# Performance work log

Measured on AMD Instinct MI355X. Metric: run time of the kernel, lower is better.

The kernel has to match this reference:

```python
import jax, jax.numpy as jnp
import numpy as np

EPS = 1e-5
KH = KW = 3
PAD = 1

def conv3x3(x, w, b=None):
    out = jax.lax.conv_general_dilated(
        x, w, window_strides=(1, 1), padding=((PAD, PAD), (PAD, PAD)),
        dimension_numbers=("NCHW", "OIHW", "NCHW"))
    if b is not None:
        out = out + b[None, :, None, None]
    return out

def batchnorm(x, gamma, beta):
    # training-mode BatchNorm2d: batch statistics over (N, H, W)
    mean = x.mean(axis=(0, 2, 3), keepdims=True)
    var = x.var(axis=(0, 2, 3), keepdims=True)
    return gamma[None, :, None, None] * (x - mean) / jnp.sqrt(var + EPS) + beta[None, :, None, None]

def bilinear_gather(x, y_pos, x_pos):
    # x: [B,C,H,W]; y_pos/x_pos: [B,P,H,W] (P = KH*KW sampling taps)
    # zero padding outside image (mmcv modulated deform conv semantics)
    B, C, H, W = x.shape
    P = y_pos.shape[1]
    x_flat = x.reshape(B, C, H * W)
    y0 = jnp.floor(y_pos)
    x0 = jnp.floor(x_pos)
    ly = y_pos - y0
    lx = x_pos - x0
    out = jnp.zeros((B, C, P, H, W), dtype=x.dtype)
    for dy, dx, wgt in ((0, 0, (1 - ly) * (1 - lx)), (0, 1, (1 - ly) * lx),
                        (1, 0, ly * (1 - lx)), (1, 1, ly * lx)):
        yi = y0 + dy
        xi = x0 + dx
        valid = ((yi >= 0) & (yi <= H - 1) & (xi >= 0) & (xi <= W - 1)).astype(x.dtype)
        yc = jnp.clip(yi, 0, H - 1).astype(jnp.int32)
        xc = jnp.clip(xi, 0, W - 1).astype(jnp.int32)
        idx = (yc * W + xc).reshape(B, 1, P * H * W)
        vals = jnp.take_along_axis(x_flat, jnp.broadcast_to(idx, (B, C, P * H * W)), axis=2)
        vals = vals.reshape(B, C, P, H, W)
        out = out + vals * (wgt * valid)[:, None]
    return out  # [B,C,P,H,W]

def modulated_deform_conv(x, w_off, b_off, w_dcn):
    B, C, H, W = x.shape
    P = KH * KW
    off = conv3x3(x, w_off, b_off)  # [B, 3*P, H, W]
    o1, o2, m = jnp.split(off, 3, axis=1)
    offset = jnp.concatenate([o1, o2], axis=1)            # [B, 2P, H, W]
    offset = offset.reshape(B, P, 2, H, W)                # channel 2p -> dy, 2p+1 -> dx
    mask = jax.nn.sigmoid(m)                              # [B, P, H, W]
    hh = jnp.arange(H, dtype=x.dtype)
    ww = jnp.arange(W, dtype=x.dtype)
    ky = jnp.arange(KH, dtype=x.dtype)
    kx = jnp.arange(KW, dtype=x.dtype)
    # base sampling grid per tap p = ky*KW + kx: (h - PAD + ky, w - PAD + kx)
    base_y = (hh[None, :] - PAD + ky[:, None])            # [KH, H]
    base_x = (ww[None, :] - PAD + kx[:, None])            # [KW, W]
    base_y = jnp.broadcast_to(base_y[:, None, :, None], (KH, KW, H, W)).reshape(P, H, W)
    base_x = jnp.broadcast_to(base_x[None, :, None, :], (KH, KW, H, W)).reshape(P, H, W)
    y_pos = base_y[None] + offset[:, :, 0]                # [B,P,H,W]
    x_pos = base_x[None] + offset[:, :, 1]
    sampled = bilinear_gather(x, y_pos, x_pos)            # [B,C,P,H,W]
    sampled = sampled * mask[:, None]
    w = w_dcn.reshape(w_dcn.shape[0], C, P)               # [O, C, P]
    return jnp.einsum("bcphw,ocp->bohw", sampled, w)

def setup_inputs() -> dict:
    key = jax.random.key(0)
    ks = jax.random.split(key, 10)
    B, Ch, H, W = 4, 256, 64, 64
    Cin, Cout = 2 * Ch, 256
    P = KH * KW
    inp = {
        "input_v": jax.random.normal(ks[0], (B, Ch, H, W), jnp.float32),
        "input_i": jax.random.normal(ks[1], (B, Ch, H, W), jnp.float32),
        "w_off": jax.random.normal(ks[2], (3 * P, Cin, KH, KW), jnp.float32) * 0.01,
        "b_off": jnp.zeros((3 * P,), jnp.float32),
        "w_dcn": jax.random.normal(ks[3], (Cout, Cin, KH, KW), jnp.float32) * (1.0 / np.sqrt(Cin * P)),
        "gamma1": jnp.ones((Cout,), jnp.float32),
        "beta1": jnp.zeros((Cout,), jnp.float32),
        "w2": jax.random.normal(ks[4], (Cout, Cout, KH, KW), jnp.float32) * (1.0 / np.sqrt(Cout * P)),
        "gamma2": jnp.ones((Cout,), jnp.float32),
        "beta2": jnp.zeros((Cout,), jnp.float32),
    }
    return inp

def reference(input_v, input_i, w_off, b_off, w_dcn, gamma1, beta1, w2, gamma2, beta2):
    x = jnp.concatenate([input_v, input_i], axis=1)
    out = modulated_deform_conv(x, w_off, b_off, w_dcn)
    out = jax.nn.relu(batchnorm(out, gamma1, beta1))
    out = jax.nn.relu(batchnorm(conv3x3(out, w2), gamma2, beta2))
    return out
```

## Files before the change

kernel.cpp:

```cpp
#include <hip/hip_runtime.h>
#include <cstdint>
#include <cstddef>

typedef unsigned short u16;
typedef __attribute__((ext_vector_type(8))) short s16x8;
typedef __attribute__((ext_vector_type(4))) float f32x4;

#define DEV __device__ __forceinline__

DEV float bf2f(short u){
  union { unsigned int i; float f; } v;
  v.i = ((unsigned int)(u16)u) << 16;
  return v.f;
}
DEV short f2bf(float f){
  union { float f; unsigned int i; } v; v.f = f;
  unsigned int u = v.i;
  u += 0x7fffu + ((u >> 16) & 1u);
  return (short)(u >> 16);
}
DEV s16x8 s16x8_zero(){
  s16x8 z;
#pragma unroll
  for(int j=0;j<8;j++) z[j]=0;
  return z;
}
DEV f32x4 f32x4_zero(){
  f32x4 z;
#pragma unroll
  for(int j=0;j<4;j++) z[j]=0.f;
  return z;
}
DEV f32x4 mfma16(s16x8 a, s16x8 b, f32x4 c){
  return __builtin_amdgcn_mfma_f32_16x16x32_bf16(a, b, c, 0, 0, 0);
}
DEV void cp16(const void* g, void* l){
  __builtin_amdgcn_global_load_lds(
      (const __attribute__((address_space(1))) unsigned int*)g,
      (__attribute__((address_space(3))) unsigned int*)l, 16, 0, 0);
}

static constexpr size_t OFF_ACC_B   = 0;
static constexpr size_t OUT1_ACC_B  = 2097152;
static constexpr size_t OUT2_ACC_B  = 18874368;
static constexpr size_t STATS_B     = 35651584;
static constexpr size_t ZERO_BYTES  = 35655680;
static constexpr size_t XN_PAD_B    = 35655680;
static constexpr size_t OUT1N_PAD_B = 53497856;
static constexpr size_t WOFFT_B     = 62418944;
static constexpr size_t WDCNT_B     = 62713856;
static constexpr size_t W2T_B       = 65073152;
static constexpr size_t SAMP_O_B    = 66252800;
static constexpr size_t SAMP_W_B    = 68612096;

__global__ void k_border(u16* __restrict__ xp, u16* __restrict__ op){
  const int cid = blockIdx.x, t = threadIdx.x;
  const int b = cid / 260, rem = cid % 260;
  int y, x;
  if(rem < 132){ y = (rem/66)*65; x = rem%66; }
  else { int r2 = rem-132; x = (r2>>6)*65; y = 1 + (r2&63); }
  const size_t cell = (size_t)(b*66+y)*66 + x;
  ((unsigned int*)(xp + cell*512))[t] = 0;
  if(t < 128) ((unsigned int*)(op + cell*256))[t] = 0;
}

__global__ void k_x_to_nhwc(const float* __restrict__ v, const float* __restrict__ vi,
                            u16* __restrict__ xn){
  __shared__ float tile[64][65];
  const int b = blockIdx.z, c0 = blockIdx.y*64, h = blockIdx.x;
  const float* src = (c0 < 256) ? (v  + ((size_t)b*256 + c0)      *4096)
                                : (vi + ((size_t)b*256 + (c0-256))*4096);
  const int t = threadIdx.x;
#pragma unroll
  for(int k=0;k<16;k++){
    int idx = t + k*256;
    int cl = idx >> 6, wl = idx & 63;
    tile[cl][wl] = src[(size_t)cl*4096 + h*64 + wl];
  }
  __syncthreads();
#pragma unroll
  for(int k=0;k<16;k++){
    int idx = t + k*256;
    int wl = idx >> 6, cl = idx & 63;
    xn[((size_t)(b*66 + h+1)*66 + (wl+1))*512 + c0 + cl] = (u16)f2bf(tile[cl][wl]);
  }
}

__global__ void k_prep_woff(const float* __restrict__ w, u16* __restrict__ wt){
  int idx = blockIdx.x*256 + threadIdx.x;
  if(idx >= 32*4608) return;
  int n = idx / 4608, k = idx % 4608;
  int t = k >> 9, c = k & 511;
  float val = (n < 27) ? w[(size_t)(n*512 + c)*9 + t] : 0.f;
  wt[idx] = (u16)f2bf(val);
}
__global__ void k_prep_wdcn(const float* __restrict__ w, u16* __restrict__ wt){
  int idx = blockIdx.x*256 + threadIdx.x;
  if(idx >= 256*4608) return;
  int n = idx / 4608, k = idx % 4608;
  int t = k >> 9, c = k & 511;
  wt[idx] = (u16)f2bf(w[(size_t)(n*512 + c)*9 + t]);
}
__global__ void k_prep_w2(const float* __restrict__ w, u16* __restrict__ wt){
  int idx = blockIdx.x*256 + threadIdx.x;
  if(idx >= 256*2304) return;
  int n = idx / 2304, k = idx % 2304;
  int t = k >> 8, c = k & 255;
  wt[idx] = (u16)f2bf(w[(size_t)(n*256 + c)*9 + t]);
}

__global__ __launch_bounds__(256, 4) void k_conv_off(
    const u16* __restrict__ xn, const u16* __restrict__ wt, float* __restrict__ offa){
  __shared__ short A_lds[8][64][8];
  __shared__ short B_lds[8][32][8];
  const int tid = threadIdx.x;
  const int lane = tid & 63, wid = tid >> 6;
  const int quad = lane >> 4, ln = lane & 15;
  const int m0 = blockIdx.x * 64;
  const int b = m0 >> 12;
  const int h = (m0 >> 6) & 63;
  const int ks = blockIdx.y;
  const int m_base = wid * 16;
  const s16x8* Ap = (const s16x8*)A_lds;
  const s16x8* Bp = (const s16x8*)B_lds;
  f32x4 acc[2];
  acc[0] = f32x4_zero(); acc[1] = f32x4_zero();

  for(int tpi=0; tpi<3; tpi++){
    const int tp = ks*3 + tpi;
    const int ty = tp/3, tx = tp - ty*3;
    const u16* arow = xn + ((size_t)(b*66 + h+ty)*66 + lane + tx)*512;
    const u16* brow = wt + (size_t)(lane & 31)*4608 + tp*512 + (wid*2 + (lane>>5))*8;
    for(int s=0; s<8; s++){
      const int cb = s*64;
      cp16(arow + cb + (wid*2)*8,     &A_lds[wid*2][0][0]);
      cp16(arow + cb + (wid*2+1)*8,   &A_lds[wid*2+1][0][0]);
      cp16(brow + cb,                 &B_lds[wid*2][0][0]);
      __syncthreads();
#pragma unroll
      for(int cc=0; cc<2; cc++){
        const int s2 = cc*4 + quad;
        s16x8 a  = Ap[s2*64 + m_base + ln];
        s16x8 b0 = Bp[s2*32 + ln];
        s16x8 b1 = Bp[s2*32 + 16 + ln];
        acc[0] = mfma16(a, b0, acc[0]);
        acc[1] = mfma16(a, b1, acc[1]);
      }
      __syncthreads();
    }
  }
#pragma unroll
  for(int nf=0;nf<2;nf++){
    const int col = nf*16 + ln;
#pragma unroll
    for(int i=0;i<4;i++){
      const int row = m_base + quad*4 + i;
      unsafeAtomicAdd(offa + (size_t)(m0+row)*32 + col, acc[nf][i]);
    }
  }
}

__global__ void k_sampler(const float* __restrict__ offa, const float* __restrict__ boff,
                          int* __restrict__ so, float* __restrict__ sw){
  const int idx = blockIdx.x*256 + threadIdx.x;
  if(idx >= 16384*9) return;
  const int m = idx / 9, tp = idx - m*9;
  const int b = m >> 12, h = (m >> 6) & 63, w = m & 63;
  const float* orow = offa + (size_t)m*32;
  float dy = orow[2*tp]   + boff[2*tp];
  float dx = orow[2*tp+1] + boff[2*tp+1];
  float mz = orow[18+tp]  + boff[18+tp];
  float mk = 1.f / (1.f + expf(-mz));
  float ypos = (float)(h - 1 + tp/3) + dy;
  float xpos = (float)(w - 1 + tp%3) + dx;
  float y0f = floorf(ypos), x0f = floorf(xpos);
  float ly = ypos - y0f, lx = xpos - x0f;
  int y0 = (int)y0f, x0 = (int)x0f;
#pragma unroll
  for(int k=0;k<4;k++){
    int ddy = k >> 1, ddx = k & 1;
    int yi = y0 + ddy, xi = x0 + ddx;
    bool vv = (yi >= 0) & (yi < 64) & (xi >= 0) & (xi < 64);
    float wk = (ddy ? ly : 1.f-ly) * (ddx ? lx : 1.f-lx) * mk;
    if(!vv) wk = 0.f;
    int yc = yi < 0 ? 0 : (yi > 63 ? 63 : yi);
    int xc = xi < 0 ? 0 : (xi > 63 ? 63 : xi);
    so[(size_t)idx*4 + k] = ((b*66 + yc+1)*66 + xc+1) << 9;
    sw[(size_t)idx*4 + k] = wk;
  }
}

__global__ __launch_bounds__(256, 3) void k_dcn(
    const u16* __restrict__ xn, const u16* __restrict__ wt,
    const int* __restrict__ so, const float* __restrict__ sw,
    float* __restrict__ outa){
  __shared__ short A_lds[8][64][8];
  __shared__ short B_lds[8][256][8];
  const int tid = threadIdx.x;
  const int lane = tid & 63, wid = tid >> 6;
  const int quad = lane >> 4, ln = lane & 15;
  const int m0 = blockIdx.x * 64;
  const int ks = blockIdx.y;
  const int m_base = (wid >> 1)*32, n_base = (wid & 1)*128;
  const int r = tid >> 2, sub = tid & 3;
  const int nw = wid * 64;
  const s16x8* Ap = (const s16x8*)A_lds;
  const s16x8* Bp = (const s16x8*)B_lds;
  f32x4 acc[2][8];
#pragma unroll
  for(int mf=0;mf<2;mf++)
#pragma unroll
    for(int nf=0;nf<8;nf++) acc[mf][nf] = f32x4_zero();

  for(int tpi=0; tpi<3; tpi++){
    const int tp = ks*3 + tpi;
    const int4   po = *(const int4*)  (so + ((size_t)(m0+r)*9 + tp)*4);
    const float4 pw = *(const float4*)(sw + ((size_t)(m0+r)*9 + tp)*4);
    const u16* a0p = xn + po.x + sub*8;
    const u16* a1p = xn + po.y + sub*8;
    const u16* a2p = xn + po.z + sub*8;
    const u16* a3p = xn + po.w + sub*8;
    const u16* bsrc = wt + (size_t)(nw + lane)*4608 + tp*512;

    for(int s=0; s<8; s++){
      const int c0 = s*64;
      s16x8 v00 = *(const s16x8*)(a0p + c0);
      s16x8 v01 = *(const s16x8*)(a1p + c0);
      s16x8 v02 = *(const s16x8*)(a2p + c0);
      s16x8 v03 = *(const s16x8*)(a3p + c0);
      s16x8 v10 = *(const s16x8*)(a0p + c0 + 32);
      s16x8 v11 = *(const s16x8*)(a1p + c0 + 32);
      s16x8 v12 = *(const s16x8*)(a2p + c0 + 32);
      s16x8 v13 = *(const s16x8*)(a3p + c0 + 32);
#pragma unroll
      for(int s2=0; s2<8; s2++)
        cp16(bsrc + c0 + s2*8, &B_lds[s2][nw][0]);
      s16x8 pk0, pk1;
#pragma unroll
      for(int j=0;j<8;j++){
        float f0 = pw.x * bf2f(v00[j]);
        f0 = fmaf(pw.y, bf2f(v01[j]), f0);
        f0 = fmaf(pw.z, bf2f(v02[j]), f0);
        f0 = fmaf(pw.w, bf2f(v03[j]), f0);
        pk0[j] = f2bf(f0);
        float f1 = pw.x * bf2f(v10[j]);
        f1 = fmaf(pw.y, bf2f(v11[j]), f1);
        f1 = fmaf(pw.z, bf2f(v12[j]), f1);
        f1 = fmaf(pw.w, bf2f(v13[j]), f1);
        pk1[j] = f2bf(f1);
      }
      *(s16x8*)(&A_lds[sub][r][0])     = pk0;
      *(s16x8*)(&A_lds[sub+4][r][0])   = pk1;
      __syncthreads();
#pragma unroll
      for(int cc=0; cc<2; cc++){
        const int s2 = cc*4 + quad;
        s16x8 a0 = Ap[s2*64 + m_base + ln];
        s16x8 a1 = Ap[s2*64 + m_base + 16 + ln];
        s16x8 bfr[8];
#pragma unroll
        for(int nf=0;nf<8;nf++) bfr[nf] = Bp[s2*256 + n_base + nf*16 + ln];
#pragma unroll
        for(int nf=0;nf<8;nf++){
          acc[0][nf] = mfma16(a0, bfr[nf], acc[0][nf]);
          acc[1][nf] = mfma16(a1, bfr[nf], acc[1][nf]);
        }
      }
      __syncthreads();
    }
  }
#pragma unroll
  for(int mf=0;mf<2;mf++)
#pragma unroll
    for(int nf=0;nf<8;nf++){
      const int col = n_base + nf*16 + ln;
#pragma unroll
      for(int i=0;i<4;i++){
        const int row = m_base + mf*16 + quad*4 + i;
        unsafeAtomicAdd(outa + (size_t)(m0+row)*256 + col, acc[mf][nf][i]);
      }
    }
}

__global__ __launch_bounds__(256, 3) void k_conv2(
    const u16* __restrict__ a_in, const u16* __restrict__ wt, float* __restrict__ outa){
  __shared__ short A_lds[8][64][8];
  __shared__ short B_lds[8][256][8];
  const int tid = threadIdx.x;
  const int lane = tid & 63, wid = tid >> 6;
  const int quad = lane >> 4, ln = lane & 15;
  const int m0 = blockIdx.x * 64;
  const int b = m0 >> 12;
  const int h = (m0 >> 6) & 63;
  const int ks = blockIdx.y;
  const int m_base = (wid >> 1)*32, n_base = (wid & 1)*128;
  const int nw = wid * 64;
  const s16x8* Ap = (const s16x8*)A_lds;
  const s16x8* Bp = (const s16x8*)B_lds;
  f32x4 acc[2][8];
#pragma unroll
  for(int mf=0;mf<2;mf++)
#pragma unroll
    for(int nf=0;nf<8;nf++) acc[mf][nf] = f32x4_zero();

  for(int tpi=0; tpi<3; tpi++){
    const int tp = ks*3 + tpi;
    const int ty = tp/3, tx = tp - ty*3;
    const u16* arow = a_in + ((size_t)(b*66 + h+ty)*66 + lane + tx)*256;
    const u16* bsrc = wt + (size_t)(nw + lane)*2304 + tp*256;
    for(int s=0; s<4; s++){
      const int c0 = s*64;
      cp16(arow + c0 + wid*8,       &A_lds[wid][0][0]);
      cp16(arow + c0 + (wid+4)*8,   &A_lds[wid+4][0][0]);
#pragma unroll
      for(int s2=0; s2<8; s2++)
        cp16(bsrc + c0 + s2*8, &B_lds[s2][nw][0]);
      __syncthreads();
#pragma unroll
      for(int cc=0; cc<2; cc++){
        const int s2 = cc*4 + quad;
        s16x8 a0 = Ap[s2*64 + m_base + ln];
        s16x8 a1 = Ap[s2*64 + m_base + 16 + ln];
        s16x8 bfr[8];
#pragma unroll
        for(int nf=0;nf<8;nf++) bfr[nf] = Bp[s2*256 + n_base + nf*16 + ln];
#pragma unroll
        for(int nf=0;nf<8;nf++){
          acc[0][nf] = mfma16(a0, bfr[nf], acc[0][nf]);
          acc[1][nf] = mfma16(a1, bfr[nf], acc[1][nf]);
        }
      }
      __syncthreads();
    }
  }
#pragma unroll
  for(int mf=0;mf<2;mf++)
#pragma unroll
    for(int nf=0;nf<8;nf++){
      const int col = n_base + nf*16 + ln;
#pragma unroll
      for(int i=0;i<4;i++){
        const int row = m_base + mf*16 + quad*4 + i;
        unsafeAtomicAdd(outa + (size_t)(m0+row)*256 + col, acc[mf][nf][i]);
      }
    }
}

__global__ void k_stats(const float* __restrict__ acc, float* __restrict__ sum,
                        float* __restrict__ sq){
  const int m0 = blockIdx.x*64;
  const int c = threadIdx.x;
  float s = 0.f, q = 0.f;
  for(int i=0;i<64;i++){
    float v = acc[(size_t)(m0+i)*256 + c];
    s += v; q += v*v;
  }
  unsafeAtomicAdd(sum + c, s);
  unsafeAtomicAdd(sq + c, q);
}

__global__ void k_bn1(const float* __restrict__ acc, const float* __restrict__ sum,
                      const float* __restrict__ sq, const float* __restrict__ g,
                      const float* __restrict__ bt, u16* __restrict__ o){
  __shared__ float sc[256], sh[256];
  const int t = threadIdx.x;
  {
    float mean = sum[t] * (1.f/16384.f);
    float var  = sq[t] * (1.f/16384.f) - mean*mean;
    float rstd = rsqrtf(var + 1e-5f);
    float s = g[t] * rstd;
    sc[t] = s; sh[t] = bt[t] - mean*s;
  }
  __syncthreads();
  const int c4 = (t & 63) * 4;
  const float s0 = sc[c4], s1 = sc[c4+1], s2 = sc[c4+2], s3 = sc[c4+3];
  const float h0 = sh[c4], h1 = sh[c4+1], h2 = sh[c4+2], h3 = sh[c4+3];
#pragma unroll
  for(int k=0;k<4;k++){
    int m = blockIdx.x*16 + k*4 + (t>>6);
    int b = m >> 12, hh = (m >> 6) & 63, ww = m & 63;
    const float4 v = *(const float4*)(acc + (size_t)m*256 + c4);
    unsigned int lo = (unsigned int)(u16)f2bf(fmaxf(0.f, v.x*s0 + h0))
                    | ((unsigned int)(u16)f2bf(fmaxf(0.f, v.y*s1 + h1)) << 16);
    unsigned int hi = (unsigned int)(u16)f2bf(fmaxf(0.f, v.z*s2 + h2))
                    | ((unsigned int)(u16)f2bf(fmaxf(0.f, v.w*s3 + h3)) << 16);
    uint2 pr; pr.x = lo; pr.y = hi;
    *(uint2*)(o + ((size_t)(b*66 + hh+1)*66 + ww+1)*256 + c4) = pr;
  }
}

__global__ void k_bn2_out(const float* __restrict__ acc, const float* __restrict__ sum,
                          const float* __restrict__ sq, const float* __restrict__ g,
                          const float* __restrict__ bt, float* __restrict__ out){
  __shared__ float tile[64][65];
  __shared__ float sc[64], sh[64];
  const int t = threadIdx.x;
  const int b = blockIdx.z, c0 = blockIdx.y*64, hw0 = blockIdx.x*64;
  if(t < 64){
    int c = c0 + t;
    float mean = sum[c] * (1.f/16384.f);
    float var  = sq[c] * (1.f/16384.f) - mean*mean;
    float rstd = rsqrtf(var + 1e-5f);
    float s = g[c] * rstd;
    sc[t] = s; sh[t] = bt[c] - mean*s;
  }
  __syncthreads();
#pragma unroll
  for(int k=0;k<16;k++){
    int idx = t + k*256;
    int wl = idx >> 6, cl = idx & 63;
    float v = acc[(size_t)((b<<12) + hw0 + wl)*256 + c0 + cl];
    tile[wl][cl] = fmaxf(0.f, v*sc[cl] + sh[cl]);
  }
  __syncthreads();
#pragma unroll
  for(int k=0;k<16;k++){
    int idx = t + k*256;
    int cl = idx >> 6, wl = idx & 63;
    out[(size_t)(b*256 + c0 + cl)*4096 + hw0 + wl] = tile[wl][cl];
  }
}

extern "C" void kernel_launch(void* const* d_in, const int* in_sizes, int n_in,
                              void* d_out, int out_size, void* d_ws, size_t ws_size,
                              hipStream_t stream){
  const float* in_v  = (const float*)d_in[0];
  const float* in_i  = (const float*)d_in[1];
  const float* w_off = (const float*)d_in[2];
  const float* b_off = (const float*)d_in[3];
  const float* w_dcn = (const float*)d_in[4];
  const float* g1    = (const float*)d_in[5];
  const float* bt1   = (const float*)d_in[6];
  const float* w2    = (const float*)d_in[7];
  const float* g2    = (const float*)d_in[8];
  const float* bt2   = (const float*)d_in[9];
  float* out = (float*)d_out;
  char* ws = (char*)d_ws;

  float* off_acc  = (float*)(ws + OFF_ACC_B);
  float* out1_acc = (float*)(ws + OUT1_ACC_B);
  float* out2_acc = (float*)(ws + OUT2_ACC_B);
  float* stats    = (float*)(ws + STATS_B);
  float* sum1 = stats,       *sq1 = stats + 256;
  float* sum2 = stats + 512, *sq2 = stats + 768;
  u16* xn_pad    = (u16*)(ws + XN_PAD_B);
  u16* out1n_pad = (u16*)(ws + OUT1N_PAD_B);
  u16* wofft = (u16*)(ws + WOFFT_B);
  u16* wdcnt = (u16*)(ws + WDCNT_B);
  u16* w2t   = (u16*)(ws + W2T_B);
  int*   samp_o = (int*)(ws + SAMP_O_B);
  float* samp_w = (float*)(ws + SAMP_W_B);

  hipMemsetAsync(ws, 0, ZERO_BYTES, stream);
  k_border<<<1040, 256, 0, stream>>>(xn_pad, out1n_pad);
  k_x_to_nhwc<<<dim3(64,8,4), 256, 0, stream>>>(in_v, in_i, xn_pad);
  k_prep_woff<<<576, 256, 0, stream>>>(w_off, wofft);
  k_prep_wdcn<<<4608, 256, 0, stream>>>(w_dcn, wdcnt);
  k_prep_w2<<<2304, 256, 0, stream>>>(w2, w2t);
  k_conv_off<<<dim3(256,3), 256, 0, stream>>>(xn_pad, wofft, off_acc);
  k_sampler<<<576, 256, 0, stream>>>(off_acc, b_off, samp_o, samp_w);
  k_dcn<<<dim3(256,3), 256, 0, stream>>>(xn_pad, wdcnt, samp_o, samp_w, out1_acc);
  k_stats<<<256, 256, 0, stream>>>(out1_acc, sum1, sq1);
  k_bn1<<<1024, 256, 0, stream>>>(out1_acc, sum1, sq1, g1, bt1, out1n_pad);
  k_conv2<<<dim3(256,3), 256, 0, stream>>>(out1n_pad, w2t, out2_acc);
  k_stats<<<256, 256, 0, stream>>>(out2_acc, sum2, sq2);
  k_bn2_out<<<dim3(64,4,4), 256, 0, stream>>>(out2_acc, sum2, sq2, g2, bt2, out);
}
```

Baseline: 411.1 us.

## Double-buffer LDS in conv GEMMs, retile weights, split K into six slices

The three implicit-GEMM conv kernels (offset conv, deformable conv, conv2) now use ping-pong LDS buffers with a 32-channel K step. The next tile's global loads and bilinear gather are issued before the current tile's MFMAs, cutting the barriers per step from two to one. Weights are pre-permuted into a K-chunk-major, N-contiguous layout so each B tile is one contiguous copy. The K split doubles from 3 to 6 grid slices and the occupancy hints rise. In exchange there are more atomic adds into the fp32 accumulators and more register pressure from keeping prefetched gather values live.

```diff
diff --git a/kernel.cpp b/kernel.cpp
--- a/kernel.cpp
+++ b/kernel.cpp
@@ -18,12 +18,6 @@
   unsigned int u = v.i;
   u += 0x7fffu + ((u >> 16) & 1u);
   return (short)(u >> 16);
-}
-DEV s16x8 s16x8_zero(){
-  s16x8 z;
-#pragma unroll
-  for(int j=0;j<8;j++) z[j]=0;
-  return z;
 }
 DEV f32x4 f32x4_zero(){
   f32x4 z;
@@ -87,75 +81,82 @@
 }
 
 __global__ void k_prep_woff(const float* __restrict__ w, u16* __restrict__ wt){
-  int idx = blockIdx.x*256 + threadIdx.x;
-  if(idx >= 32*4608) return;
-  int n = idx / 4608, k = idx % 4608;
-  int t = k >> 9, c = k & 511;
-  float val = (n < 27) ? w[(size_t)(n*512 + c)*9 + t] : 0.f;
-  wt[idx] = (u16)f2bf(val);
+  int i = blockIdx.x*256 + threadIdx.x;
+  if(i >= 147456) return;
+  int j = i & 7, n = (i>>3) & 31, kcp = i>>8;
+  int kc = kcp & 63, tp = kcp >> 6;
+  int c = kc*8 + j;
+  float val = (n < 27) ? w[(size_t)(n*512 + c)*9 + tp] : 0.f;
+  wt[i] = (u16)f2bf(val);
 }
 __global__ void k_prep_wdcn(const float* __restrict__ w, u16* __restrict__ wt){
-  int idx = blockIdx.x*256 + threadIdx.x;
-  if(idx >= 256*4608) return;
-  int n = idx / 4608, k = idx % 4608;
-  int t = k >> 9, c = k & 511;
-  wt[idx] = (u16)f2bf(w[(size_t)(n*512 + c)*9 + t]);
+  int i = blockIdx.x*256 + threadIdx.x;
+  if(i >= 1179648) return;
+  int j = i & 7, n = (i>>3) & 255, kcp = i>>11;
+  int kc = kcp & 63, tp = kcp >> 6;
+  int c = kc*8 + j;
+  wt[i] = (u16)f2bf(w[(size_t)(n*512 + c)*9 + tp]);
 }
 __global__ void k_prep_w2(const float* __restrict__ w, u16* __restrict__ wt){
-  int idx = blockIdx.x*256 + threadIdx.x;
-  if(idx >= 256*2304) return;
-  int n = idx / 2304, k = idx % 2304;
-  int t = k >> 8, c = k & 255;
-  wt[idx] = (u16)f2bf(w[(size_t)(n*256 + c)*9 + t]);
-}
-
-__global__ __launch_bounds__(256, 4) void k_conv_off(
+  int i = blockIdx.x*256 + threadIdx.x;
+  if(i >= 589824) return;
+  int j = i & 7, n = (i>>3) & 255, kcp = i>>11;
+  int kc = kcp & 31, tp = kcp >> 5;
+  int c = kc*8 + j;
+  wt[i] = (u16)f2bf(w[(size_t)(n*256 + c)*9 + tp]);
+}
+
+__global__ __launch_bounds__(256, 6) void k_conv_off(
     const u16* __restrict__ xn, const u16* __restrict__ wt, float* __restrict__ offa){
-  __shared__ short A_lds[8][64][8];
-  __shared__ short B_lds[8][32][8];
+  __shared__ short A[2][4][64][8];
+  __shared__ short B[2][4][32][8];
   const int tid = threadIdx.x;
   const int lane = tid & 63, wid = tid >> 6;
   const int quad = lane >> 4, ln = lane & 15;
   const int m0 = blockIdx.x * 64;
-  const int b = m0 >> 12;
-  const int h = (m0 >> 6) & 63;
-  const int ks = blockIdx.y;
+  const int b = m0 >> 12, h = (m0 >> 6) & 63;
+  const int gst0 = blockIdx.y * 24;
   const int m_base = wid * 16;
-  const s16x8* Ap = (const s16x8*)A_lds;
-  const s16x8* Bp = (const s16x8*)B_lds;
-  f32x4 acc[2];
-  acc[0] = f32x4_zero(); acc[1] = f32x4_zero();
-
-  for(int tpi=0; tpi<3; tpi++){
-    const int tp = ks*3 + tpi;
+  f32x4 acc0 = f32x4_zero(), acc1 = f32x4_zero();
+
+  {
+    const int tp = gst0 >> 4, s = gst0 & 15;
     const int ty = tp/3, tx = tp - ty*3;
-    const u16* arow = xn + ((size_t)(b*66 + h+ty)*66 + lane + tx)*512;
-    const u16* brow = wt + (size_t)(lane & 31)*4608 + tp*512 + (wid*2 + (lane>>5))*8;
-    for(int s=0; s<8; s++){
-      const int cb = s*64;
-      cp16(arow + cb + (wid*2)*8,     &A_lds[wid*2][0][0]);
-      cp16(arow + cb + (wid*2+1)*8,   &A_lds[wid*2+1][0][0]);
-      cp16(brow + cb,                 &B_lds[wid*2][0][0]);
-      __syncthreads();
-#pragma unroll
-      for(int cc=0; cc<2; cc++){
-        const int s2 = cc*4 + quad;
-        s16x8 a  = Ap[s2*64 + m_base + ln];
-        s16x8 b0 = Bp[s2*32 + ln];
-        s16x8 b1 = Bp[s2*32 + 16 + ln];
-        acc[0] = mfma16(a, b0, acc[0]);
-        acc[1] = mfma16(a, b1, acc[1]);
-      }
-      __syncthreads();
-    }
+    cp16(xn + ((size_t)(b*66 + h+ty)*66 + lane + tx)*512 + s*32 + wid*8, &A[0][wid][0][0]);
+    if(wid < 2)
+      cp16(wt + ((size_t)tp*64 + s*4)*256 + wid*512 + lane*8, (short*)&B[0][0][0][0] + wid*512);
+  }
+  __syncthreads();
+
+  int buf = 0;
+  for(int it=0; it<24; it++){
+    const int nb = buf ^ 1;
+    if(it < 23){
+      const int gn = gst0 + it + 1;
+      const int tp = gn >> 4, s = gn & 15;
+      const int ty = tp/3, tx = tp - ty*3;
+      cp16(xn + ((size_t)(b*66 + h+ty)*66 + lane + tx)*512 + s*32 + wid*8, &A[nb][wid][0][0]);
+      if(wid < 2)
+        cp16(wt + ((size_t)tp*64 + s*4)*256 + wid*512 + lane*8, (short*)&B[nb][0][0][0] + wid*512);
+    }
+    const s16x8* Ap = (const s16x8*)&A[buf][0][0][0];
+    const s16x8* Bp = (const s16x8*)&B[buf][0][0][0];
+    s16x8 a  = Ap[quad*64 + m_base + ln];
+    s16x8 b0 = Bp[quad*32 + ln];
+    s16x8 b1 = Bp[quad*32 + 16 + ln];
+    acc0 = mfma16(a, b0, acc0);
+    acc1 = mfma16(a, b1, acc1);
+    __syncthreads();
+    buf = nb;
   }
 #pragma unroll
   for(int nf=0;nf<2;nf++){
+    const f32x4 v = nf ? acc1 : acc0;
     const int col = nf*16 + ln;
 #pragma unroll
     for(int i=0;i<4;i++){
       const int row = m_base + quad*4 + i;
-      unsafeAtomicAdd(offa + (size_t)(m0+row)*32 + col, acc[nf][i]);
+      unsafeAtomicAdd(offa + (size_t)(m0+row)*32 + col, v[i]);
     }
   }
 }
@@ -190,84 +191,100 @@
   }
 }
 
-__global__ __launch_bounds__(256, 3) void k_dcn(
+__global__ __launch_bounds__(256, 4) void k_dcn(
     const u16* __restrict__ xn, const u16* __restrict__ wt,
     const int* __restrict__ so, const float* __restrict__ sw,
     float* __restrict__ outa){
-  __shared__ short A_lds[8][64][8];
-  __shared__ short B_lds[8][256][8];
+  __shared__ short A[2][4][64][8];
+  __shared__ short B[2][4][256][8];
   const int tid = threadIdx.x;
   const int lane = tid & 63, wid = tid >> 6;
   const int quad = lane >> 4, ln = lane & 15;
   const int m0 = blockIdx.x * 64;
-  const int ks = blockIdx.y;
+  const int gst0 = blockIdx.y * 24;
   const int m_base = (wid >> 1)*32, n_base = (wid & 1)*128;
   const int r = tid >> 2, sub = tid & 3;
-  const int nw = wid * 64;
-  const s16x8* Ap = (const s16x8*)A_lds;
-  const s16x8* Bp = (const s16x8*)B_lds;
   f32x4 acc[2][8];
 #pragma unroll
   for(int mf=0;mf<2;mf++)
 #pragma unroll
     for(int nf=0;nf<8;nf++) acc[mf][nf] = f32x4_zero();
 
-  for(int tpi=0; tpi<3; tpi++){
-    const int tp = ks*3 + tpi;
-    const int4   po = *(const int4*)  (so + ((size_t)(m0+r)*9 + tp)*4);
-    const float4 pw = *(const float4*)(sw + ((size_t)(m0+r)*9 + tp)*4);
-    const u16* a0p = xn + po.x + sub*8;
-    const u16* a1p = xn + po.y + sub*8;
-    const u16* a2p = xn + po.z + sub*8;
-    const u16* a3p = xn + po.w + sub*8;
-    const u16* bsrc = wt + (size_t)(nw + lane)*4608 + tp*512;
-
-    for(int s=0; s<8; s++){
-      const int c0 = s*64;
-      s16x8 v00 = *(const s16x8*)(a0p + c0);
-      s16x8 v01 = *(const s16x8*)(a1p + c0);
-      s16x8 v02 = *(const s16x8*)(a2p + c0);
-      s16x8 v03 = *(const s16x8*)(a3p + c0);
-      s16x8 v10 = *(const s16x8*)(a0p + c0 + 32);
-      s16x8 v11 = *(const s16x8*)(a1p + c0 + 32);
-      s16x8 v12 = *(const s16x8*)(a2p + c0 + 32);
-      s16x8 v13 = *(const s16x8*)(a3p + c0 + 32);
-#pragma unroll
-      for(int s2=0; s2<8; s2++)
-        cp16(bsrc + c0 + s2*8, &B_lds[s2][nw][0]);
-      s16x8 pk0, pk1;
+  int4 po; float4 pw;
+  s16x8 g0, g1, g2, g3;
+
+  {
+    const int tp = gst0 >> 4, s = gst0 & 15;
+    po = *(const int4*)  (so + ((size_t)(m0+r)*9 + tp)*4);
+    pw = *(const float4*)(sw + ((size_t)(m0+r)*9 + tp)*4);
+    const u16* bs = wt + ((size_t)tp*64 + s*4)*2048 + (wid*4)*512 + lane*8;
+    short* bd = (short*)&B[0][0][0][0] + (wid*4)*512;
+#pragma unroll
+    for(int i=0;i<4;i++) cp16(bs + i*512, bd + i*512);
+    const int c0 = s*32 + sub*8;
+    g0 = *(const s16x8*)(xn + po.x + c0);
+    g1 = *(const s16x8*)(xn + po.y + c0);
+    g2 = *(const s16x8*)(xn + po.z + c0);
+    g3 = *(const s16x8*)(xn + po.w + c0);
+    s16x8 pk;
+#pragma unroll
+    for(int j=0;j<8;j++){
+      float f = pw.x * bf2f(g0[j]);
+      f = fmaf(pw.y, bf2f(g1[j]), f);
+      f = fmaf(pw.z, bf2f(g2[j]), f);
+      f = fmaf(pw.w, bf2f(g3[j]), f);
+      pk[j] = f2bf(f);
+    }
+    *(s16x8*)(&A[0][sub][r][0]) = pk;
+  }
+  __syncthreads();
+
+  int buf = 0;
+  for(int it=0; it<24; it++){
+    const int nb = buf ^ 1;
+    if(it < 23){
+      const int gn = gst0 + it + 1;
+      const int tp = gn >> 4, s = gn & 15;
+      if((gn & 15) == 0){
+        po = *(const int4*)  (so + ((size_t)(m0+r)*9 + tp)*4);
+        pw = *(const float4*)(sw + ((size_t)(m0+r)*9 + tp)*4);
+      }
+      const u16* bs = wt + ((size_t)tp*64 + s*4)*2048 + (wid*4)*512 + lane*8;
+      short* bd = (short*)&B[nb][0][0][0] + (wid*4)*512;
+#pragma unroll
+      for(int i=0;i<4;i++) cp16(bs + i*512, bd + i*512);
+      const int c0 = s*32 + sub*8;
+      g0 = *(const s16x8*)(xn + po.x + c0);
+      g1 = *(const s16x8*)(xn + po.y + c0);
+      g2 = *(const s16x8*)(xn + po.z + c0);
+      g3 = *(const s16x8*)(xn + po.w + c0);
+    }
+    {
+      const s16x8* Ap = (const s16x8*)&A[buf][0][0][0];
+      const s16x8* Bp = (const s16x8*)&B[buf][0][0][0];
+      s16x8 a0 = Ap[quad*64 + m_base + ln];
+      s16x8 a1 = Ap[quad*64 + m_base + 16 + ln];
+#pragma unroll
+      for(int nf=0;nf<8;nf++){
+        s16x8 bf = Bp[quad*256 + n_base + nf*16 + ln];
+        acc[0][nf] = mfma16(a0, bf, acc[0][nf]);
+        acc[1][nf] = mfma16(a1, bf, acc[1][nf]);
+      }
+    }
+    if(it < 23){
+      s16x8 pk;
 #pragma unroll
       for(int j=0;j<8;j++){
-        float f0 = pw.x * bf2f(v00[j]);
-        f0 = fmaf(pw.y, bf2f(v01[j]), f0);
-        f0 = fmaf(pw.z, bf2f(v02[j]), f0);
-        f0 = fmaf(pw.w, bf2f(v03[j]), f0);
-        pk0[j] = f2bf(f0);
-        float f1 = pw.x * bf2f(v10[j]);
-        f1 = fmaf(pw.y, bf2f(v11[j]), f1);
-        f1 = fmaf(pw.z, bf2f(v12[j]), f1);
-        f1 = fmaf(pw.w, bf2f(v13[j]), f1);
-        pk1[j] = f2bf(f1);
+        float f = pw.x * bf2f(g0[j]);
+        f = fmaf(pw.y, bf2f(g1[j]), f);
+        f = fmaf(pw.z, bf2f(g2[j]), f);
+        f = fmaf(pw.w, bf2f(g3[j]), f);
+        pk[j] = f2bf(f);
       }
-      *(s16x8*)(&A_lds[sub][r][0])     = pk0;
-      *(s16x8*)(&A_lds[sub+4][r][0])   = pk1;
-      __syncthreads();
-#pragma unroll
-      for(int cc=0; cc<2; cc++){
-        const int s2 = cc*4 + quad;
-        s16x8 a0 = Ap[s2*64 + m_base + ln];
-        s16x8 a1 = Ap[s2*64 + m_base + 16 + ln];
-        s16x8 bfr[8];
-#pragma unroll
-        for(int nf=0;nf<8;nf++) bfr[nf] = Bp[s2*256 + n_base + nf*16 + ln];
-#pragma unroll
-        for(int nf=0;nf<8;nf++){
-          acc[0][nf] = mfma16(a0, bfr[nf], acc[0][nf]);
-          acc[1][nf] = mfma16(a1, bfr[nf], acc[1][nf]);
-        }
-      }
-      __syncthreads();
-    }
+      *(s16x8*)(&A[nb][sub][r][0]) = pk;
+    }
+    __syncthreads();
+    buf = nb;
   }
 #pragma unroll
   for(int mf=0;mf<2;mf++)
@@ -282,56 +299,59 @@
     }
 }
 
-__global__ __launch_bounds__(256, 3) void k_conv2(
+__global__ __launch_bounds__(256, 4) void k_conv2(
     const u16* __restrict__ a_in, const u16* __restrict__ wt, float* __restrict__ outa){
-  __shared__ short A_lds[8][64][8];
-  __shared__ short B_lds[8][256][8];
+  __shared__ short A[2][4][64][8];
+  __shared__ short B[2][4][256][8];
   const int tid = threadIdx.x;
   const int lane = tid & 63, wid = tid >> 6;
   const int quad = lane >> 4, ln = lane & 15;
   const int m0 = blockIdx.x * 64;
-  const int b = m0 >> 12;
-  const int h = (m0 >> 6) & 63;
-  const int ks = blockIdx.y;
+  const int b = m0 >> 12, h = (m0 >> 6) & 63;
+  const int gst0 = blockIdx.y * 12;
   const int m_base = (wid >> 1)*32, n_base = (wid & 1)*128;
-  const int nw = wid * 64;
-  const s16x8* Ap = (const s16x8*)A_lds;
-  const s16x8* Bp = (const s16x8*)B_lds;
   f32x4 acc[2][8];
 #pragma unroll
   for(int mf=0;mf<2;mf++)
 #pragma unroll
     for(int nf=0;nf<8;nf++) acc[mf][nf] = f32x4_zero();
 
-  for(int tpi=0; tpi<3; tpi++){
-    const int tp = ks*3 + tpi;
+  {
+    const int tp = gst0 >> 3, s = gst0 & 7;
     const int ty = tp/3, tx = tp - ty*3;
-    const u16* arow = a_in + ((size_t)(b*66 + h+ty)*66 + lane + tx)*256;
-    const u16* bsrc = wt + (size_t)(nw + lane)*2304 + tp*256;
-    for(int s=0; s<4; s++){
-      const int c0 = s*64;
-      cp16(arow + c0 + wid*8,       &A_lds[wid][0][0]);
-      cp16(arow + c0 + (wid+4)*8,   &A_lds[wid+4][0][0]);
-#pragma unroll
-      for(int s2=0; s2<8; s2++)
-        cp16(bsrc + c0 + s2*8, &B_lds[s2][nw][0]);
-      __syncthreads();
-#pragma unroll
-      for(int cc=0; cc<2; cc++){
-        const int s2 = cc*4 + quad;
-        s16x8 a0 = Ap[s2*64 + m_base + ln];
-        s16x8 a1 = Ap[s2*64 + m_base + 16 + ln];
-        s16x8 bfr[8];
-#pragma unroll
-        for(int nf=0;nf<8;nf++) bfr[nf] = Bp[s2*256 + n_base + nf*16 + ln];
-#pragma unroll
-        for(int nf=0;nf<8;nf++){
-          acc[0][nf] = mfma16(a0, bfr[nf], acc[0][nf]);
-          acc[1][nf] = mfma16(a1, bfr[nf], acc[1][nf]);
-        }
-      }
-      __syncthreads();
-    }
+    cp16(a_in + ((size_t)(b*66 + h+ty)*66 + lane + tx)*256 + s*32 + wid*8, &A[0][wid][0][0]);
+    const u16* bs = wt + ((size_t)tp*32 + s*4)*2048 + (wid*4)*512 + lane*8;
+    short* bd = (short*)&B[0][0][0][0] + (wid*4)*512;
+#pragma unroll
+    for(int i=0;i<4;i++) cp16(bs + i*512, bd + i*512);
+  }
+  __syncthreads();
+
+  int buf = 0;
+  for(int it=0; it<12; it++){
+    const int nb = buf ^ 1;
+    if(it < 11){
+      const int gn = gst0 + it + 1;
+      const int tp = gn >> 3, s = gn & 7;
+      const int ty = tp/3, tx = tp - ty*3;
+      cp16(a_in + ((size_t)(b*66 + h+ty)*66 + lane + tx)*256 + s*32 + wid*8, &A[nb][wid][0][0]);
+      const u16* bs = wt + ((size_t)tp*32 + s*4)*2048 + (wid*4)*512 + lane*8;
+      short* bd = (short*)&B[nb][0][0][0] + (wid*4)*512;
+#pragma unroll
+      for(int i=0;i<4;i++) cp16(bs + i*512, bd + i*512);
+    }
+    const s16x8* Ap = (const s16x8*)&A[buf][0][0][0];
+    const s16x8* Bp = (const s16x8*)&B[buf][0][0][0];
+    s16x8 a0 = Ap[quad*64 + m_base + ln];
+    s16x8 a1 = Ap[quad*64 + m_base + 16 + ln];
+#pragma unroll
+    for(int nf=0;nf<8;nf++){
+      s16x8 bf = Bp[quad*256 + n_base + nf*16 + ln];
+      acc[0][nf] = mfma16(a0, bf, acc[0][nf]);
+      acc[1][nf] = mfma16(a1, bf, acc[1][nf]);
+    }
+    __syncthreads();
+    buf = nb;
   }
 #pragma unroll
   for(int mf=0;mf<2;mf++)
@@ -457,12 +477,12 @@
   k_prep_woff<<<576, 256, 0, stream>>>(w_off, wofft);
   k_prep_wdcn<<<4608, 256, 0, stream>>>(w_dcn, wdcnt);
   k_prep_w2<<<2304, 256, 0, stream>>>(w2, w2t);
-  k_conv_off<<<dim3(256,3), 256, 0, stream>>>(xn_pad, wofft, off_acc);
+  k_conv_off<<<dim3(256,6), 256, 0, stream>>>(xn_pad, wofft, off_acc);
   k_sampler<<<576, 256, 0, stream>>>(off_acc, b_off, samp_o, samp_w);
-  k_dcn<<<dim3(256,3), 256, 0, stream>>>(xn_pad, wdcnt, samp_o, samp_w, out1_acc);
+  k_dcn<<<dim3(256,6), 256, 0, stream>>>(xn_pad, wdcnt, samp_o, samp_w, out1_acc);
   k_stats<<<256, 256, 0, stream>>>(out1_acc, sum1, sq1);
   k_bn1<<<1024, 256, 0, stream>>>(out1_acc, sum1, sq1, g1, bt1, out1n_pad);
-  k_conv2<<<dim3(256,3), 256, 0, stream>>>(out1n_pad, w2t, out2_acc);
+  k_conv2<<<dim3(256,6), 256, 0, stream>>>(out1n_pad, w2t, out2_acc);
   k_stats<<<256, 256, 0, stream>>>(out2_acc, sum2, sq2);
   k_bn2_out<<<dim3(64,4,4), 256, 0, stream>>>(out2_acc, sum2, sq2, g2, bt2, out);
 }
```

Measured after the change: 407.5 us. About the same (-0.9%).
